# Performance work log

Hardware: AMD Instinct MI355X
Metric: run time of the kernel (lower is better)

The kernel has to match this reference:

```python
import jax, jax.numpy as jnp
import numpy as np

N, E, H, C = 10000, 160000, 7, 64
NEG_SLOPE = 0.2


def setup_inputs() -> dict:
    key = jax.random.key(0)
    ks = iter(jax.random.split(key, 32))
    def w(shape, fan_in):
        return jax.random.normal(next(ks), shape, jnp.float32) * (1.0 / np.sqrt(fan_in))
    inp = {
        "x": jax.random.normal(next(ks), (N, 1024), jnp.float32),
        "edge_index": jax.random.randint(next(ks), (2, E), 0, N, jnp.int64),
        # input MLP 1024->512->256->64
        "W1": w((1024, 512), 1024), "b1": jnp.zeros((512,), jnp.float32),
        "W2": w((512, 256), 512),   "b2": jnp.zeros((256,), jnp.float32),
        "W3": w((256, 64), 256),    "b3": jnp.zeros((64,), jnp.float32),
        # 5 stacked GATv2Conv(64,64,heads=7,concat=False) layers
        "Wl": w((5, 64, H * C), 64), "bl": jnp.zeros((5, H * C), jnp.float32),
        "Wr": w((5, 64, H * C), 64),
        "att": w((5, H, C), C),
        "cbias": jnp.zeros((5, C), jnp.float32),
        # output MLP 64->32->16->9
        "V1": w((64, 32), 64), "c1": jnp.zeros((32,), jnp.float32),
        "V2": w((32, 16), 32), "c2": jnp.zeros((16,), jnp.float32),
        "V3": w((16, 9), 16),  "c3": jnp.zeros((9,), jnp.float32),
    }
    return inp


def _gatv2_conv(x, src, dst, Wl, bl, Wr, att, bias):
    # x: [N,64]; src/dst: [E'] (self-loops already appended)
    xl = (x @ Wl + bl).reshape(N, H, C)   # lin_l (with bias)
    xr = (x @ Wr).reshape(N, H, C)        # lin_r (no bias)
    e = jax.nn.leaky_relu(xl[src] + xr[dst], NEG_SLOPE)      # [E',H,C]
    logits = jnp.einsum('ehc,hc->eh', e, att)                # [E',H]
    m = jax.ops.segment_max(logits, dst, num_segments=N)     # [N,H]
    a = jnp.exp(logits - m[dst])
    s = jax.ops.segment_sum(a, dst, num_segments=N)          # [N,H]
    alpha = a / (s[dst] + 1e-16)                             # ragged softmax per dst node
    out = jax.ops.segment_sum(alpha[:, :, None] * xl[src], dst, num_segments=N)  # [N,H,C]
    return out.mean(axis=1) + bias                           # concat=False -> mean heads


def reference(x, edge_index, W1, b1, W2, b2, W3, b3, Wl, bl, Wr, att, cbias,
              V1, c1, V2, c2, V3, c3):
    # GATv2Conv adds self-loops by default
    loops = jnp.arange(N, dtype=edge_index.dtype)
    src = jnp.concatenate([edge_index[0], loops])
    dst = jnp.concatenate([edge_index[1], loops])

    h = jax.nn.relu(x @ W1 + b1)
    h = jax.nn.relu(h @ W2 + b2)
    h = jax.nn.relu(h @ W3 + b3)
    for l in range(5):
        h = jax.nn.relu(_gatv2_conv(h, src, dst, Wl[l], bl[l], Wr[l], att[l], cbias[l]))
    h = jax.nn.relu(h) @ V1 + c1
    h = jax.nn.relu(h) @ V2 + c2
    h = jax.nn.relu(h) @ V3 + c3
    return jax.nn.log_softmax(h, axis=1)
```

## Files before the change

kernel.cpp:

```cpp
#include <hip/hip_runtime.h>
#include <hip/hip_bf16.h>
#include <math.h>

#define NNODES 10000
#define NEDGES 160000
#define ETOT (NEDGES + NNODES)
#define HEADS 7
#define CH 64
#define HC 448
#define HCP 1024

typedef __attribute__((ext_vector_type(8))) short short8;
typedef __attribute__((ext_vector_type(4))) float floatx4;

__device__ __forceinline__ float bf_lo(unsigned u) {
  return __uint_as_float(u << 16);
}
__device__ __forceinline__ float bf_hi(unsigned u) {
  return __uint_as_float(u & 0xffff0000u);
}
__device__ __forceinline__ short f2bf(float v) {
  return __bfloat16_as_short(__float2bfloat16(v));
}

#define P0 2560000
#define P1 (P0 + 512 * 1024)
#define P2 (P1 + 256 * 512)
#define P3 (P2 + 64 * 256)
#define P4 (P3 + 5 * HCP * 64)
#define P5 (P4 + 5 * HCP)
#define P6 (P5 + NNODES)
#define PTOT P6

__global__ __launch_bounds__(256) void prep_kernel(
    const float* __restrict__ x, short* __restrict__ xb,
    const float* __restrict__ W1, short* __restrict__ W1t,
    const float* __restrict__ W2, short* __restrict__ W2t,
    const float* __restrict__ W3, short* __restrict__ W3t,
    const float* __restrict__ Wl, const float* __restrict__ Wr,
    const float* __restrict__ bl, short* __restrict__ Wgt,
    float* __restrict__ bg, int* __restrict__ cnt) {
  int idx = blockIdx.x * 256 + threadIdx.x;
  if (idx < P0) {
    float4 v = *(const float4*)&x[(size_t)idx * 4];
    short4 o;
    o.x = f2bf(v.x); o.y = f2bf(v.y); o.z = f2bf(v.z); o.w = f2bf(v.w);
    *(short4*)&xb[(size_t)idx * 4] = o;
  } else if (idx < P1) {
    int i = idx - P0;
    int n = i / 1024, k = i % 1024;
    W1t[i] = f2bf(W1[(size_t)k * 512 + n]);
  } else if (idx < P2) {
    int i = idx - P1;
    int n = i / 512, k = i % 512;
    W2t[i] = f2bf(W2[(size_t)k * 256 + n]);
  } else if (idx < P3) {
    int i = idx - P2;
    int n = i / 256, k = i % 256;
    W3t[i] = f2bf(W3[(size_t)k * 64 + n]);
  } else if (idx < P4) {
    int i = idx - P3;
    int l = i / (HCP * 64);
    int rem = i % (HCP * 64);
    int col = rem / 64, k = rem % 64;
    int half = col >> 9;
    int within = col & 511;
    int c = within >> 3, h = within & 7;
    float v = 0.f;
    if (h < 7) {
      const float* W = half ? Wr : Wl;
      v = W[((size_t)l * 64 + k) * HC + h * 64 + c];
    }
    Wgt[i] = f2bf(v);
  } else if (idx < P5) {
    int i = idx - P4;
    int l = i >> 10, col = i & 1023;
    int half = col >> 9, within = col & 511;
    int c = within >> 3, h = within & 7;
    bg[i] = (!half && h < 7) ? bl[(size_t)l * HC + h * 64 + c] : 0.f;
  } else if (idx < P6) {
    cnt[idx - P5] = 1;
  }
}

template <int BM, int BN, int RELU>
__global__ __launch_bounds__(256) void mfma_gemm(
    const short* __restrict__ A, const short* __restrict__ Bt,
    const float* __restrict__ bias, short* __restrict__ C,
    int M, int K, int Nc) {
  __shared__ short As[BM * 64];
  __shared__ short Bs[BN * 64];
  constexpr int MI = BM / 32;
  constexpr int NJ = BN / 32;
  int tid = threadIdx.x;
  int lane = tid & 63, wave = tid >> 6;
  int wm = wave >> 1, wn = wave & 1;
  int row0 = blockIdx.x * BM, col0 = blockIdx.y * BN;
  floatx4 acc[MI][NJ] = {};

  for (int k0 = 0; k0 < K; k0 += 64) {
    #pragma unroll
    for (int i = 0; i < BM / 32; ++i) {
      int c = i * 4 + wave;
      int r = c * 8 + (lane >> 3);
      int k = (lane & 7) * 8;
      int grow = row0 + r;
      if (grow >= M) grow = M - 1;
      __builtin_amdgcn_global_load_lds(
          (const __attribute__((address_space(1))) void*)(A + (size_t)grow * K + k0 + k),
          (__attribute__((address_space(3))) void*)(As + c * 512), 16, 0, 0);
    }
    #pragma unroll
    for (int i = 0; i < BN / 32; ++i) {
      int c = i * 4 + wave;
      int r = c * 8 + (lane >> 3);
      int k = (lane & 7) * 8;
      int gcol = col0 + r;
      if (gcol >= Nc) gcol = Nc - 1;
      __builtin_amdgcn_global_load_lds(
          (const __attribute__((address_space(1))) void*)(Bt + (size_t)gcol * K + k0 + k),
          (__attribute__((address_space(3))) void*)(Bs + c * 512), 16, 0, 0);
    }
    __syncthreads();
    int lr = lane & 15, lq = lane >> 4;
    #pragma unroll
    for (int kk = 0; kk < 64; kk += 32) {
      short8 af[MI], bf[NJ];
      #pragma unroll
      for (int i = 0; i < MI; ++i)
        af[i] = *(const short8*)&As[(wm * (BM / 2) + i * 16 + lr) * 64 + kk + lq * 8];
      #pragma unroll
      for (int j = 0; j < NJ; ++j)
        bf[j] = *(const short8*)&Bs[(wn * (BN / 2) + j * 16 + lr) * 64 + kk + lq * 8];
      #pragma unroll
      for (int i = 0; i < MI; ++i)
        #pragma unroll
        for (int j = 0; j < NJ; ++j)
          acc[i][j] = __builtin_amdgcn_mfma_f32_16x16x32_bf16(
              af[i], bf[j], acc[i][j], 0, 0, 0);
    }
    __syncthreads();
  }

  int lr = lane & 15, lq = lane >> 4;
  #pragma unroll
  for (int j = 0; j < NJ; ++j) {
    int col = col0 + wn * (BN / 2) + j * 16 + lr;
    float bj = bias ? bias[col] : 0.f;
    #pragma unroll
    for (int i = 0; i < MI; ++i) {
      int rbase = row0 + wm * (BM / 2) + i * 16 + lq * 4;
      #pragma unroll
      for (int r = 0; r < 4; ++r) {
        int row = rbase + r;
        if (row < M) {
          float v = acc[i][j][r] + bj;
          if (RELU) v = fmaxf(v, 0.f);
          C[(size_t)row * Nc + col] = f2bf(v);
        }
      }
    }
  }
}

__global__ void hist_kernel(const int* __restrict__ ei, int* __restrict__ cnt) {
  int e = blockIdx.x * 256 + threadIdx.x;
  if (e < NEDGES) atomicAdd(&cnt[ei[NEDGES + e]], 1);
}

__global__ __launch_bounds__(1024) void scan_kernel(
    const int* __restrict__ cnt, int* __restrict__ row_start,
    int* __restrict__ cursor) {
  __shared__ int wsum[16];
  int t = threadIdx.x;
  int lane = t & 63, w = t >> 6;
  int base = t * 10;
  int v[10], s = 0;
  #pragma unroll
  for (int i = 0; i < 10; ++i) {
    v[i] = (base + i < NNODES) ? cnt[base + i] : 0;
    s += v[i];
  }
  int incl = s;
  #pragma unroll
  for (int off = 1; off < 64; off <<= 1) {
    int o = __shfl_up(incl, off, 64);
    if (lane >= off) incl += o;
  }
  if (lane == 63) wsum[w] = incl;
  __syncthreads();
  if (w == 0) {
    int wv = (lane < 16) ? wsum[lane] : 0;
    #pragma unroll
    for (int off = 1; off < 16; off <<= 1) {
      int o = __shfl_up(wv, off, 64);
      if (lane >= off) wv += o;
    }
    if (lane < 16) wsum[lane] = wv;
  }
  __syncthreads();
  int woff = (w > 0) ? wsum[w - 1] : 0;
  int excl = woff + incl - s;
  #pragma unroll
  for (int i = 0; i < 10; ++i) {
    if (base + i < NNODES) {
      row_start[base + i] = excl;
      cursor[base + i] = excl;
    }
    excl += v[i];
  }
  if (t == 1023) row_start[NNODES] = wsum[15];
}

__global__ void scatter_kernel(const int* __restrict__ ei,
                               int* __restrict__ cursor,
                               int* __restrict__ csr_src) {
  int t = blockIdx.x * 256 + threadIdx.x;
  if (t < NNODES) {
    int pos = atomicAdd(&cursor[t], 1);
    csr_src[pos] = t;
  } else if (t < ETOT) {
    int e = t - NNODES;
    int d = ei[NEDGES + e];
    int pos = atomicAdd(&cursor[d], 1);
    csr_src[pos] = ei[e];
  }
}

template <int FINAL>
__global__ __launch_bounds__(256) void gat_fused_kernel(
    const short* __restrict__ xlt, const float* __restrict__ att,
    const float* __restrict__ cbias, const int* __restrict__ row_start,
    const int* __restrict__ csr_src, short* __restrict__ hout,
    const float* __restrict__ V1, const float* __restrict__ c1,
    const float* __restrict__ V2, const float* __restrict__ c2,
    const float* __restrict__ V3, const float* __restrict__ c3,
    float* __restrict__ out) {
  __shared__ float att_s[512];
  __shared__ float part[2][14][64];
  __shared__ float wlds[4][8][8];
  __shared__ int   slds[4][8];
  __shared__ float hb[2][64], r1[2][32], r2[2][16], z3[2][9];

  for (int i = threadIdx.x; i < 512; i += 256) {
    int c = i >> 3, h = i & 7;
    att_s[i] = (h < 7) ? att[h * 64 + c] : 0.f;
  }
  __syncthreads();

  int lane = threadIdx.x & 63;
  int wv = threadIdx.x >> 6;
  int nw = wv >> 1;
  int half = wv & 1;
  int n = blockIdx.x * 2 + nw;
  int beg = row_start[n], end = row_start[n + 1];
  int t0c = end - beg - half;
  int cnt = (t0c > 0) ? ((t0c + 1) >> 1) : 0;

  int le = lane >> 3, cl = lane & 7;
  const uint4* xrp = (const uint4*)(xlt + (size_t)n * HCP + 512);

  float o0 = 0.f, o1 = 0.f, o2 = 0.f, o3 = 0.f, o4 = 0.f, o5 = 0.f, o6 = 0.f;
  float s0 = 0.f, s1 = 0.f, s2 = 0.f, s3 = 0.f, s4 = 0.f, s5 = 0.f, s6 = 0.f;

  for (int i0 = 0; i0 < cnt; i0 += 8) {
    int idx = i0 + le;
    int ide = (idx < cnt) ? idx : (cnt - 1);
    int e = beg + half + 2 * ide;
    int src = csr_src[e];
    if (cl == 0) slds[wv][le] = src;
    const uint4* xlp = (const uint4*)(xlt + (size_t)src * HCP);
    float acc[7] = {0.f, 0.f, 0.f, 0.f, 0.f, 0.f, 0.f};
    #pragma unroll
    for (int q = 0; q < 8; ++q) {
      int c = q * 8 + cl;
      uint4 a = xlp[c];
      uint4 b = xrp[c];
      float4 t0 = *(const float4*)&att_s[c * 8];
      float4 t1 = *(const float4*)&att_s[c * 8 + 4];
      float e0v = bf_lo(a.x) + bf_lo(b.x);
      float e1v = bf_hi(a.x) + bf_hi(b.x);
      float e2v = bf_lo(a.y) + bf_lo(b.y);
      float e3v = bf_hi(a.y) + bf_hi(b.y);
      float e4v = bf_lo(a.z) + bf_lo(b.z);
      float e5v = bf_hi(a.z) + bf_hi(b.z);
      float e6v = bf_lo(a.w) + bf_lo(b.w);
      e0v = fmaxf(e0v, 0.2f * e0v); e1v = fmaxf(e1v, 0.2f * e1v);
      e2v = fmaxf(e2v, 0.2f * e2v); e3v = fmaxf(e3v, 0.2f * e3v);
      e4v = fmaxf(e4v, 0.2f * e4v); e5v = fmaxf(e5v, 0.2f * e5v);
      e6v = fmaxf(e6v, 0.2f * e6v);
      acc[0] += t0.x * e0v; acc[1] += t0.y * e1v;
      acc[2] += t0.z * e2v; acc[3] += t0.w * e3v;
      acc[4] += t1.x * e4v; acc[5] += t1.y * e5v;
      acc[6] += t1.z * e6v;
    }
    #pragma unroll
    for (int h = 0; h < 7; ++h) {
      acc[h] += __shfl_xor(acc[h], 1, 64);
      acc[h] += __shfl_xor(acc[h], 2, 64);
      acc[h] += __shfl_xor(acc[h], 4, 64);
    }
    float res = 0.f;
    #pragma unroll
    for (int h = 0; h < 7; ++h) res = (cl == h) ? acc[h] : res;
    wlds[wv][le][cl] = (cl < 7) ? __expf(res) : 0.f;
    asm volatile("" ::: "memory");

    int m = cnt - i0;
    if (m > 8) m = 8;
    #pragma unroll 4
    for (int j = 0; j < m; ++j) {
      int src2 = slds[wv][j];
      float4 wa = *(const float4*)&wlds[wv][j][0];
      float4 wb = *(const float4*)&wlds[wv][j][4];
      uint4 xv = *(const uint4*)(xlt + (size_t)src2 * HCP + (size_t)lane * 8);
      o0 += wa.x * bf_lo(xv.x);
      o1 += wa.y * bf_hi(xv.x);
      o2 += wa.z * bf_lo(xv.y);
      o3 += wa.w * bf_hi(xv.y);
      o4 += wb.x * bf_lo(xv.z);
      o5 += wb.y * bf_hi(xv.z);
      o6 += wb.z * bf_lo(xv.w);
      s0 += wa.x; s1 += wa.y; s2 += wa.z; s3 += wa.w;
      s4 += wb.x; s5 += wb.y; s6 += wb.z;
    }
    asm volatile("" ::: "memory");
  }

  if (half == 1) {
    part[nw][0][lane] = o0;  part[nw][1][lane] = o1;
    part[nw][2][lane] = o2;  part[nw][3][lane] = o3;
    part[nw][4][lane] = o4;  part[nw][5][lane] = o5;
    part[nw][6][lane] = o6;
    part[nw][7][lane] = s0;  part[nw][8][lane] = s1;
    part[nw][9][lane] = s2;  part[nw][10][lane] = s3;
    part[nw][11][lane] = s4; part[nw][12][lane] = s5;
    part[nw][13][lane] = s6;
  }
  __syncthreads();
  if (half == 0) {
    o0 += part[nw][0][lane];  o1 += part[nw][1][lane];
    o2 += part[nw][2][lane];  o3 += part[nw][3][lane];
    o4 += part[nw][4][lane];  o5 += part[nw][5][lane];
    o6 += part[nw][6][lane];
    s0 += part[nw][7][lane];  s1 += part[nw][8][lane];
    s2 += part[nw][9][lane];  s3 += part[nw][10][lane];
    s4 += part[nw][11][lane]; s5 += part[nw][12][lane];
    s6 += part[nw][13][lane];
    float accv = o0 / (s0 + 1e-16f) + o1 / (s1 + 1e-16f) + o2 / (s2 + 1e-16f) +
                 o3 / (s3 + 1e-16f) + o4 / (s4 + 1e-16f) + o5 / (s5 + 1e-16f) +
                 o6 / (s6 + 1e-16f);
    float v = fmaxf(accv * (1.0f / 7.0f) + cbias[lane], 0.f);
    if (!FINAL) {
      hout[(size_t)n * 64 + lane] = f2bf(v);
    } else {
      int t = lane;
      hb[nw][t] = v;
      if (t < 32) {
        float a = c1[t];
        #pragma unroll
        for (int k = 0; k < 64; ++k) a += hb[nw][k] * V1[k * 32 + t];
        r1[nw][t] = fmaxf(a, 0.f);
      }
      if (t < 16) {
        float a = c2[t];
        #pragma unroll
        for (int k = 0; k < 32; ++k) a += r1[nw][k] * V2[k * 16 + t];
        r2[nw][t] = fmaxf(a, 0.f);
      }
      if (t < 9) {
        float a = c3[t];
        #pragma unroll
        for (int k = 0; k < 16; ++k) a += r2[nw][k] * V3[k * 9 + t];
        z3[nw][t] = a;
      }
      if (t < 9) {
        float mx = z3[nw][0];
        #pragma unroll
        for (int k = 1; k < 9; ++k) mx = fmaxf(mx, z3[nw][k]);
        float s = 0.f;
        #pragma unroll
        for (int k = 0; k < 9; ++k) s += __expf(z3[nw][k] - mx);
        out[(size_t)n * 9 + t] = z3[nw][t] - mx - logf(s);
      }
    }
  }
}

extern "C" void kernel_launch(void* const* d_in, const int* in_sizes, int n_in,
                              void* d_out, int out_size, void* d_ws, size_t ws_size,
                              hipStream_t stream) {
  const float* x   = (const float*)d_in[0];
  const int*   ei  = (const int*)d_in[1];
  const float* W1  = (const float*)d_in[2];
  const float* b1  = (const float*)d_in[3];
  const float* W2  = (const float*)d_in[4];
  const float* b2  = (const float*)d_in[5];
  const float* W3  = (const float*)d_in[6];
  const float* b3  = (const float*)d_in[7];
  const float* Wl  = (const float*)d_in[8];
  const float* bl  = (const float*)d_in[9];
  const float* Wr  = (const float*)d_in[10];
  const float* att = (const float*)d_in[11];
  const float* cb  = (const float*)d_in[12];
  const float* V1  = (const float*)d_in[13];
  const float* c1  = (const float*)d_in[14];
  const float* V2  = (const float*)d_in[15];
  const float* c2  = (const float*)d_in[16];
  const float* V3  = (const float*)d_in[17];
  const float* c3  = (const float*)d_in[18];
  float* out = (float*)d_out;

  char* ws = (char*)d_ws;
  size_t off = 0;
  auto alloc = [&](size_t bytes) {
    void* p = ws + off;
    off = (off + bytes + 255) & ~(size_t)255;
    return p;
  };
  char* region0 = (char*)alloc((size_t)NNODES * 1024 * 2 + 1024);
  short* xb  = (short*)region0;
  short* h2  = (short*)region0;
  short* xlt = (short*)region0;
  char* region1 = (char*)alloc((size_t)NNODES * 512 * 2 + 1024);
  short* h1 = (short*)region1;
  short* hA = (short*)region1;
  short* hB = hA + (size_t)NNODES * 64;
  short* W1t = (short*)alloc((size_t)512 * 1024 * 2);
  short* W2t = (short*)alloc((size_t)256 * 512 * 2);
  short* W3t = (short*)alloc((size_t)64 * 256 * 2);
  short* Wgt = (short*)alloc((size_t)5 * HCP * 64 * 2);
  float* bg  = (float*)alloc((size_t)5 * HCP * 4);
  int* cnt       = (int*)alloc((size_t)NNODES * 4);
  int* row_start = (int*)alloc((size_t)(NNODES + 1) * 4);
  int* cursor    = (int*)alloc((size_t)NNODES * 4);
  int* csr_src   = (int*)alloc((size_t)ETOT * 4);

  prep_kernel<<<(PTOT + 255) / 256, 256, 0, stream>>>(
      x, xb, W1, W1t, W2, W2t, W3, W3t, Wl, Wr, bl, Wgt, bg, cnt);

  hist_kernel<<<(NEDGES + 255) / 256, 256, 0, stream>>>(ei, cnt);
  scan_kernel<<<1, 1024, 0, stream>>>(cnt, row_start, cursor);
  scatter_kernel<<<(ETOT + 255) / 256, 256, 0, stream>>>(ei, cursor, csr_src);

  mfma_gemm<64, 128, 1><<<dim3(157, 4), 256, 0, stream>>>(
      xb, W1t, b1, h1, NNODES, 1024, 512);
  mfma_gemm<64, 128, 1><<<dim3(157, 2), 256, 0, stream>>>(
      h1, W2t, b2, h2, NNODES, 512, 256);
  mfma_gemm<64, 64, 1><<<dim3(157, 1), 256, 0, stream>>>(
      h2, W3t, b3, hA, NNODES, 256, 64);

  short* hcur = hA;
  short* hnext = hB;
  for (int layer = 0; layer < 5; ++layer) {
    mfma_gemm<128, 128, 0><<<dim3(79, 8), 256, 0, stream>>>(
        hcur, Wgt + (size_t)layer * HCP * 64, bg + (size_t)layer * HCP, xlt,
        NNODES, 64, HCP);
    if (layer < 4) {
      gat_fused_kernel<0><<<5000, 256, 0, stream>>>(
          xlt, att + (size_t)layer * HC, cb + (size_t)layer * 64, row_start,
          csr_src, hnext, V1, c1, V2, c2, V3, c3, out);
    } else {
      gat_fused_kernel<1><<<5000, 256, 0, stream>>>(
          xlt, att + (size_t)layer * HC, cb + (size_t)layer * 64, row_start,
          csr_src, hnext, V1, c1, V2, c2, V3, c3, out);
    }
    short* tmp = hcur; hcur = hnext; hnext = tmp;
  }
}
```

Measured before the change: 579.9 us.

## Use one wave per node and reuse loaded source rows for aggregation

Each wave now handles a whole destination node instead of two waves splitting its edges. The source xl row loaded for the attention logit is kept in registers and reused for the weighted aggregation, which removes the second global gather and the LDS staging of weights and indices. Per-lane partial sums are combined with cross-lane shuffles at the end, so the block-level partial buffer and the __syncthreads go away. The xr row and the next batch of source indices are preloaded. The cost is much higher register use (56 output accumulators plus 8 uint4 loads per lane), which may lower occupancy.

```diff
diff --git a/kernel.cpp b/kernel.cpp
--- a/kernel.cpp
+++ b/kernel.cpp
@@ -237,10 +237,7 @@
     const float* __restrict__ V3, const float* __restrict__ c3,
     float* __restrict__ out) {
   __shared__ float att_s[512];
-  __shared__ float part[2][14][64];
-  __shared__ float wlds[4][8][8];
-  __shared__ int   slds[4][8];
-  __shared__ float hb[2][64], r1[2][32], r2[2][16], z3[2][9];
+  __shared__ float hb[4][64], r1[4][32], r2[4][16], z3[4][9];
 
   for (int i = threadIdx.x; i < 512; i += 256) {
     int c = i >> 3, h = i & 7;
@@ -250,41 +247,52 @@
 
   int lane = threadIdx.x & 63;
   int wv = threadIdx.x >> 6;
-  int nw = wv >> 1;
-  int half = wv & 1;
-  int n = blockIdx.x * 2 + nw;
+  int n = blockIdx.x * 4 + wv;
+  int le = lane >> 3, cl = lane & 7;
   int beg = row_start[n], end = row_start[n + 1];
-  int t0c = end - beg - half;
-  int cnt = (t0c > 0) ? ((t0c + 1) >> 1) : 0;
-
-  int le = lane >> 3, cl = lane & 7;
+  int deg = end - beg;
+
   const uint4* xrp = (const uint4*)(xlt + (size_t)n * HCP + 512);
-
-  float o0 = 0.f, o1 = 0.f, o2 = 0.f, o3 = 0.f, o4 = 0.f, o5 = 0.f, o6 = 0.f;
-  float s0 = 0.f, s1 = 0.f, s2 = 0.f, s3 = 0.f, s4 = 0.f, s5 = 0.f, s6 = 0.f;
-
-  for (int i0 = 0; i0 < cnt; i0 += 8) {
+  uint4 xr[8];
+  #pragma unroll
+  for (int q = 0; q < 8; ++q) xr[q] = xrp[q * 8 + cl];
+
+  float o[8][7];
+  float ws[7];
+  #pragma unroll
+  for (int q = 0; q < 8; ++q)
+    #pragma unroll
+    for (int h = 0; h < 7; ++h) o[q][h] = 0.f;
+  #pragma unroll
+  for (int h = 0; h < 7; ++h) ws[h] = 0.f;
+
+  int nextsrc = csr_src[beg + ((le < deg) ? le : (deg - 1))];
+
+  for (int i0 = 0; i0 < deg; i0 += 8) {
     int idx = i0 + le;
-    int ide = (idx < cnt) ? idx : (cnt - 1);
-    int e = beg + half + 2 * ide;
-    int src = csr_src[e];
-    if (cl == 0) slds[wv][le] = src;
+    int src = nextsrc;
+    {
+      int idx2 = idx + 8;
+      int ide2 = (idx2 < deg) ? idx2 : (deg - 1);
+      nextsrc = csr_src[beg + ide2];
+    }
     const uint4* xlp = (const uint4*)(xlt + (size_t)src * HCP);
+    uint4 a[8];
+    #pragma unroll
+    for (int q = 0; q < 8; ++q) a[q] = xlp[q * 8 + cl];
+
     float acc[7] = {0.f, 0.f, 0.f, 0.f, 0.f, 0.f, 0.f};
     #pragma unroll
     for (int q = 0; q < 8; ++q) {
-      int c = q * 8 + cl;
-      uint4 a = xlp[c];
-      uint4 b = xrp[c];
-      float4 t0 = *(const float4*)&att_s[c * 8];
-      float4 t1 = *(const float4*)&att_s[c * 8 + 4];
-      float e0v = bf_lo(a.x) + bf_lo(b.x);
-      float e1v = bf_hi(a.x) + bf_hi(b.x);
-      float e2v = bf_lo(a.y) + bf_lo(b.y);
-      float e3v = bf_hi(a.y) + bf_hi(b.y);
-      float e4v = bf_lo(a.z) + bf_lo(b.z);
-      float e5v = bf_hi(a.z) + bf_hi(b.z);
-      float e6v = bf_lo(a.w) + bf_lo(b.w);
+      float4 t0 = *(const float4*)&att_s[(q * 8 + cl) * 8];
+      float4 t1 = *(const float4*)&att_s[(q * 8 + cl) * 8 + 4];
+      float e0v = bf_lo(a[q].x) + bf_lo(xr[q].x);
+      float e1v = bf_hi(a[q].x) + bf_hi(xr[q].x);
+      float e2v = bf_lo(a[q].y) + bf_lo(xr[q].y);
+      float e3v = bf_hi(a[q].y) + bf_hi(xr[q].y);
+      float e4v = bf_lo(a[q].z) + bf_lo(xr[q].z);
+      float e5v = bf_hi(a[q].z) + bf_hi(xr[q].z);
+      float e6v = bf_lo(a[q].w) + bf_lo(xr[q].w);
       e0v = fmaxf(e0v, 0.2f * e0v); e1v = fmaxf(e1v, 0.2f * e1v);
       e2v = fmaxf(e2v, 0.2f * e2v); e3v = fmaxf(e3v, 0.2f * e3v);
       e4v = fmaxf(e4v, 0.2f * e4v); e5v = fmaxf(e5v, 0.2f * e5v);
@@ -300,89 +308,85 @@
       acc[h] += __shfl_xor(acc[h], 2, 64);
       acc[h] += __shfl_xor(acc[h], 4, 64);
     }
-    float res = 0.f;
-    #pragma unroll
-    for (int h = 0; h < 7; ++h) res = (cl == h) ? acc[h] : res;
-    wlds[wv][le][cl] = (cl < 7) ? __expf(res) : 0.f;
-    asm volatile("" ::: "memory");
-
-    int m = cnt - i0;
-    if (m > 8) m = 8;
-    #pragma unroll 4
-    for (int j = 0; j < m; ++j) {
-      int src2 = slds[wv][j];
-      float4 wa = *(const float4*)&wlds[wv][j][0];
-      float4 wb = *(const float4*)&wlds[wv][j][4];
-      uint4 xv = *(const uint4*)(xlt + (size_t)src2 * HCP + (size_t)lane * 8);
-      o0 += wa.x * bf_lo(xv.x);
-      o1 += wa.y * bf_hi(xv.x);
-      o2 += wa.z * bf_lo(xv.y);
-      o3 += wa.w * bf_hi(xv.y);
-      o4 += wb.x * bf_lo(xv.z);
-      o5 += wb.y * bf_hi(xv.z);
-      o6 += wb.z * bf_lo(xv.w);
-      s0 += wa.x; s1 += wa.y; s2 += wa.z; s3 += wa.w;
-      s4 += wb.x; s5 += wb.y; s6 += wb.z;
-    }
-    asm volatile("" ::: "memory");
-  }
-
-  if (half == 1) {
-    part[nw][0][lane] = o0;  part[nw][1][lane] = o1;
-    part[nw][2][lane] = o2;  part[nw][3][lane] = o3;
-    part[nw][4][lane] = o4;  part[nw][5][lane] = o5;
-    part[nw][6][lane] = o6;
-    part[nw][7][lane] = s0;  part[nw][8][lane] = s1;
-    part[nw][9][lane] = s2;  part[nw][10][lane] = s3;
-    part[nw][11][lane] = s4; part[nw][12][lane] = s5;
-    part[nw][13][lane] = s6;
-  }
-  __syncthreads();
-  if (half == 0) {
-    o0 += part[nw][0][lane];  o1 += part[nw][1][lane];
-    o2 += part[nw][2][lane];  o3 += part[nw][3][lane];
-    o4 += part[nw][4][lane];  o5 += part[nw][5][lane];
-    o6 += part[nw][6][lane];
-    s0 += part[nw][7][lane];  s1 += part[nw][8][lane];
-    s2 += part[nw][9][lane];  s3 += part[nw][10][lane];
-    s4 += part[nw][11][lane]; s5 += part[nw][12][lane];
-    s6 += part[nw][13][lane];
-    float accv = o0 / (s0 + 1e-16f) + o1 / (s1 + 1e-16f) + o2 / (s2 + 1e-16f) +
-                 o3 / (s3 + 1e-16f) + o4 / (s4 + 1e-16f) + o5 / (s5 + 1e-16f) +
-                 o6 / (s6 + 1e-16f);
-    float v = fmaxf(accv * (1.0f / 7.0f) + cbias[lane], 0.f);
-    if (!FINAL) {
-      hout[(size_t)n * 64 + lane] = f2bf(v);
-    } else {
-      int t = lane;
-      hb[nw][t] = v;
-      if (t < 32) {
-        float a = c1[t];
-        #pragma unroll
-        for (int k = 0; k < 64; ++k) a += hb[nw][k] * V1[k * 32 + t];
-        r1[nw][t] = fmaxf(a, 0.f);
-      }
-      if (t < 16) {
-        float a = c2[t];
-        #pragma unroll
-        for (int k = 0; k < 32; ++k) a += r1[nw][k] * V2[k * 16 + t];
-        r2[nw][t] = fmaxf(a, 0.f);
-      }
-      if (t < 9) {
-        float a = c3[t];
-        #pragma unroll
-        for (int k = 0; k < 16; ++k) a += r2[nw][k] * V3[k * 9 + t];
-        z3[nw][t] = a;
-      }
-      if (t < 9) {
-        float mx = z3[nw][0];
-        #pragma unroll
-        for (int k = 1; k < 9; ++k) mx = fmaxf(mx, z3[nw][k]);
-        float s = 0.f;
-        #pragma unroll
-        for (int k = 0; k < 9; ++k) s += __expf(z3[nw][k] - mx);
-        out[(size_t)n * 9 + t] = z3[nw][t] - mx - logf(s);
-      }
+    bool valid = (idx < deg);
+    float w[7];
+    #pragma unroll
+    for (int h = 0; h < 7; ++h) {
+      float wh = valid ? __expf(acc[h]) : 0.f;
+      w[h] = wh;
+      ws[h] += wh;
+    }
+    #pragma unroll
+    for (int q = 0; q < 8; ++q) {
+      o[q][0] += w[0] * bf_lo(a[q].x);
+      o[q][1] += w[1] * bf_hi(a[q].x);
+      o[q][2] += w[2] * bf_lo(a[q].y);
+      o[q][3] += w[3] * bf_hi(a[q].y);
+      o[q][4] += w[4] * bf_lo(a[q].z);
+      o[q][5] += w[5] * bf_hi(a[q].z);
+      o[q][6] += w[6] * bf_lo(a[q].w);
+    }
+  }
+
+  #pragma unroll
+  for (int h = 0; h < 7; ++h) {
+    ws[h] += __shfl_xor(ws[h], 8, 64);
+    ws[h] += __shfl_xor(ws[h], 16, 64);
+    ws[h] += __shfl_xor(ws[h], 32, 64);
+  }
+  float rs[7];
+  #pragma unroll
+  for (int h = 0; h < 7; ++h) rs[h] = 1.f / (ws[h] + 1e-16f);
+  float pv[8];
+  #pragma unroll
+  for (int q = 0; q < 8; ++q) {
+    float v = 0.f;
+    #pragma unroll
+    for (int h = 0; h < 7; ++h) v += o[q][h] * rs[h];
+    pv[q] = v;
+  }
+  #pragma unroll
+  for (int q = 0; q < 8; ++q) {
+    pv[q] += __shfl_xor(pv[q], 8, 64);
+    pv[q] += __shfl_xor(pv[q], 16, 64);
+    pv[q] += __shfl_xor(pv[q], 32, 64);
+  }
+  float vsel = pv[0];
+  #pragma unroll
+  for (int q = 1; q < 8; ++q) vsel = (le == q) ? pv[q] : vsel;
+  float v = fmaxf(vsel * (1.0f / 7.0f) + cbias[lane], 0.f);
+
+  if (!FINAL) {
+    hout[(size_t)n * 64 + lane] = f2bf(v);
+  } else {
+    int t = lane;
+    hb[wv][t] = v;
+    if (t < 32) {
+      float a = c1[t];
+      #pragma unroll
+      for (int k = 0; k < 64; ++k) a += hb[wv][k] * V1[k * 32 + t];
+      r1[wv][t] = fmaxf(a, 0.f);
+    }
+    if (t < 16) {
+      float a = c2[t];
+      #pragma unroll
+      for (int k = 0; k < 32; ++k) a += r1[wv][k] * V2[k * 16 + t];
+      r2[wv][t] = fmaxf(a, 0.f);
+    }
+    if (t < 9) {
+      float a = c3[t];
+      #pragma unroll
+      for (int k = 0; k < 16; ++k) a += r2[wv][k] * V3[k * 9 + t];
+      z3[wv][t] = a;
+    }
+    if (t < 9) {
+      float mx = z3[wv][0];
+      #pragma unroll
+      for (int k = 1; k < 9; ++k) mx = fmaxf(mx, z3[wv][k]);
+      float s = 0.f;
+      #pragma unroll
+      for (int k = 0; k < 9; ++k) s += __expf(z3[wv][k] - mx);
+      out[(size_t)n * 9 + t] = z3[wv][t] - mx - logf(s);
     }
   }
 }
@@ -457,11 +461,11 @@
         hcur, Wgt + (size_t)layer * HCP * 64, bg + (size_t)layer * HCP, xlt,
         NNODES, 64, HCP);
     if (layer < 4) {
-      gat_fused_kernel<0><<<5000, 256, 0, stream>>>(
+      gat_fused_kernel<0><<<2500, 256, 0, stream>>>(
           xlt, att + (size_t)layer * HC, cb + (size_t)layer * 64, row_start,
           csr_src, hnext, V1, c1, V2, c2, V3, c3, out);
     } else {
-      gat_fused_kernel<1><<<5000, 256, 0, stream>>>(
+      gat_fused_kernel<1><<<2500, 256, 0, stream>>>(
           xlt, att + (size_t)layer * HC, cb + (size_t)layer * 64, row_start,
           csr_src, hnext, V1, c1, V2, c2, V3, c3, out);
     }
```

After: 780.7 us. +34.6%, slower.
